# Performance work log

Measured on AMD Instinct MI355X. Metric: run time of the kernel, lower is better.

The kernel has to match this reference:

```python
import jax, jax.numpy as jnp
import numpy as np

N_NODES = 100000
N_EDGES = 1000000
HID = 128


def setup_inputs() -> dict:
    key = jax.random.key(0)
    ks = jax.random.split(key, 13)
    s = 0.05  # small init scale for numerical sanity
    return {
        "z": jax.random.normal(ks[0], (N_NODES, HID), jnp.float32),
        "edge": jax.random.randint(ks[1], (N_EDGES, 2), 0, N_NODES, jnp.int64),
        # hadamard_mlp: Linear(HID -> HID//2), ReLU, Linear(HID//2 -> 1)
        "w_h1": jax.random.normal(ks[2], (HID // 2, HID), jnp.float32) * s,
        "b_h1": jax.random.normal(ks[3], (HID // 2,), jnp.float32) * s,
        "w_h2": jax.random.normal(ks[4], (1, HID // 2), jnp.float32) * s,
        "b_h2": jax.random.normal(ks[5], (1,), jnp.float32) * s,
        # concat_mlp: Linear(2*HID -> HID), ReLU, Linear(HID -> 1)
        "w_c1": jax.random.normal(ks[6], (HID, 2 * HID), jnp.float32) * s,
        "b_c1": jax.random.normal(ks[7], (HID,), jnp.float32) * s,
        "w_c2": jax.random.normal(ks[8], (1, HID), jnp.float32) * s,
        "b_c2": jax.random.normal(ks[9], (1,), jnp.float32) * s,
        # bilinear: weight [1, HID, HID], bias [1]
        "w_b": jax.random.normal(ks[10], (1, HID, HID), jnp.float32) * s,
        "b_b": jax.random.normal(ks[11], (1,), jnp.float32) * s,
        "strategy_weights": jnp.ones((3,), jnp.float32) / 3.0,
    }


def reference(z, edge, w_h1, b_h1, w_h2, b_h2, w_c1, b_c1, w_c2, b_c2,
              w_b, b_b, strategy_weights):
    src, dst = edge[:, 0], edge[:, 1]
    z_src = z[src]                      # [E, D] gather
    z_dst = z[dst]                      # [E, D] gather
    w = jax.nn.softmax(strategy_weights)

    # strategy 1: hadamard MLP (dropout is identity in eval)
    had = z_src * z_dst                 # [E, D]
    h = jax.nn.relu(jnp.einsum('ed,hd->eh', had, w_h1) + b_h1)
    score1 = (jnp.einsum('eh,oh->eo', h, w_h2) + b_h2)[:, 0]

    # strategy 2: concat MLP
    cat = jnp.concatenate([z_src, z_dst], axis=1)  # [E, 2D]
    c = jax.nn.relu(jnp.einsum('ed,hd->eh', cat, w_c1) + b_c1)
    score2 = (jnp.einsum('eh,oh->eo', c, w_c2) + b_c2)[:, 0]

    # strategy 3: bilinear  out_e = z_src_e^T W z_dst_e + b
    score3 = jnp.einsum('ed,df,ef->e', z_src, w_b[0], z_dst) + b_b[0]

    return w[0] * score1 + w[1] * score2 + w[2] * score3
```

## Files before the change

### kernel.cpp

```cpp
#include <hip/hip_runtime.h>
#include <hip/hip_bf16.h>

#define N_NODES 100000
#define N_EDGES 1000000
#define SRCB 384
#define DSTB 512
#define NB (N_EDGES / 16)
#define NCHUNK (N_NODES / 16)

typedef float f32x4 __attribute__((ext_vector_type(4)));
typedef float f32x2 __attribute__((ext_vector_type(2)));
typedef _Float16 f16x8 __attribute__((ext_vector_type(8)));
typedef _Float16 f16x2 __attribute__((ext_vector_type(2)));

__device__ inline f16x8 pack8(float4 a, float4 b) {
    f16x8 o;
    o[0] = (_Float16)a.x; o[1] = (_Float16)a.y; o[2] = (_Float16)a.z; o[3] = (_Float16)a.w;
    o[4] = (_Float16)b.x; o[5] = (_Float16)b.y; o[6] = (_Float16)b.z; o[7] = (_Float16)b.w;
    return o;
}
__device__ inline void mfma16(f32x4& acc, f16x8 a, f16x8 b) {
    acc = __builtin_amdgcn_mfma_f32_16x16x32_f16(a, b, acc, 0, 0, 0);
}
__device__ inline float fdot2(f16x8 a, f16x8 b, int j2, float c) {
    f16x2 pa = { a[2 * j2], a[2 * j2 + 1] };
    f16x2 pb = { b[2 * j2], b[2 * j2 + 1] };
    return __builtin_amdgcn_fdot2(pa, pb, c, false);
}
__device__ inline unsigned char f2fp8(float v) {
    int p = __builtin_amdgcn_cvt_pk_fp8_f32(v, v, 0, false);
    return (unsigned char)(p & 0xff);
}

__global__ __launch_bounds__(512) void precomp_kernel(
    const float* __restrict__ z, const float* __restrict__ w_c1,
    const float* __restrict__ b_c1, const float* __restrict__ w_b,
    unsigned char* __restrict__ Ps8, unsigned char* __restrict__ Pd8)
{
    __shared__ f16x8 wlds[3072];

    const int tid = threadIdx.x;
    const int w = tid >> 6;
    const int lane = tid & 63;
    const int r = lane & 15, g = lane >> 4;
    const int gw = blockIdx.x * 8 + w;
    const int nW = gridDim.x * 8;

    float bc1v[2][4];
#pragma unroll
    for (int t = 0; t < 2; ++t)
#pragma unroll
        for (int nt = 0; nt < 4; ++nt)
            bc1v[t][nt] = b_c1[t * 64 + nt * 16 + r];

    for (int phase = 0; phase < 2; ++phase) {
        if (phase) __syncthreads();
        for (int i = tid; i < 3072; i += 512) {
            const int r_ = i & 15, g_ = (i >> 4) & 3, kk = (i >> 6) & 3;
            const int nt = (i >> 8) & 3, t = i >> 10;
            const int c = (phase * 3 + t) * 64 + nt * 16 + r_;
            const float* wrow;
            if (c < 128)       wrow = w_c1 + (size_t)c * 256;
            else if (c < 256)  wrow = w_c1 + (size_t)(c - 128) * 256 + 128;
            else               wrow = w_b + (size_t)(c - 256) * 128;
            const int k0 = kk * 32 + g_ * 8;
            float4 f0 = *reinterpret_cast<const float4*>(wrow + k0);
            float4 f1 = *reinterpret_cast<const float4*>(wrow + k0 + 4);
            wlds[i] = pack8(f0, f1);
        }
        __syncthreads();

        const f16x8* myw = wlds + g * 16 + r;

        for (int nb = gw; nb < NCHUNK; nb += nW) {
            const int node_r = nb * 16 + r;
            const float* zp = z + (size_t)node_r * 128;
            f16x8 a[4];
#pragma unroll
            for (int kk = 0; kk < 4; ++kk) {
                const int k0 = kk * 32 + g * 8;
                float4 z0 = *reinterpret_cast<const float4*>(zp + k0);
                float4 z1 = *reinterpret_cast<const float4*>(zp + k0 + 4);
                a[kk] = pack8(z0, z1);
                if (phase == 0) {
                    *reinterpret_cast<f16x8*>(
                        Ps8 + (size_t)node_r * SRCB + 128 + k0 * 2) = a[kk];
                    int q0 = __builtin_amdgcn_cvt_pk_fp8_f32(z0.x, z0.y, 0, false);
                    q0 = __builtin_amdgcn_cvt_pk_fp8_f32(z0.z, z0.w, q0, true);
                    int q1 = __builtin_amdgcn_cvt_pk_fp8_f32(z1.x, z1.y, 0, false);
                    q1 = __builtin_amdgcn_cvt_pk_fp8_f32(z1.z, z1.w, q1, true);
                    uint2 pk; pk.x = (unsigned)q0; pk.y = (unsigned)q1;
                    *reinterpret_cast<uint2*>(
                        Pd8 + (size_t)node_r * DSTB + 384 + k0) = pk;
                }
            }
#pragma unroll
            for (int t = 0; t < 3; ++t) {
                const int ct = phase * 3 + t;
                f32x4 acc[4] = {};
#pragma unroll
                for (int kk = 0; kk < 4; ++kk) {
#pragma unroll
                    for (int nt = 0; nt < 4; ++nt)
                        mfma16(acc[nt], a[kk], myw[((t * 4 + nt) * 4 + kk) * 64]);
                }
#pragma unroll
                for (int nt = 0; nt < 4; ++nt) {
#pragma unroll
                    for (int rr = 0; rr < 4; ++rr) {
                        const int node = nb * 16 + g * 4 + rr;
                        const int c = ct * 64 + nt * 16 + r;
                        float v = acc[nt][rr];
                        if (ct < 2) {
                            v += bc1v[ct][nt];
                            Ps8[(size_t)node * SRCB + c] = f2fp8(v);
                        } else if (ct < 4) {
                            Pd8[(size_t)node * DSTB + (c - 128)] = f2fp8(v);
                        } else {
                            *reinterpret_cast<_Float16*>(
                                Pd8 + (size_t)node * DSTB + 128
                                    + (size_t)(c - 256) * 2) = (_Float16)v;
                        }
                    }
                }
            }
        }
    }
}

__global__ __launch_bounds__(256) void edge_kernel(
    const int2* __restrict__ edge2,
    const unsigned char* __restrict__ Ps8, const unsigned char* __restrict__ Pd8,
    const float* __restrict__ w_h1, const float* __restrict__ b_h1,
    const float* __restrict__ w_h2, const float* __restrict__ b_h2,
    const float* __restrict__ w_c2, const float* __restrict__ b_c2,
    const float* __restrict__ b_b, const float* __restrict__ sw,
    float* __restrict__ out)
{
    __shared__ f16x8 bwlds[1024];

    const int tid = threadIdx.x;
    for (int e = tid; e < 1024; e += 256) {
        const int r_ = e & 15, g_ = (e >> 4) & 3, kkf = (e >> 6) & 3, ntf = e >> 8;
        const float* wr = w_h1 + (size_t)(ntf * 16 + r_) * 128 + g_ * 32 + kkf * 8;
        float4 f0 = *reinterpret_cast<const float4*>(wr);
        float4 f1 = *reinterpret_cast<const float4*>(wr + 4);
        bwlds[e] = pack8(f0, f1);
    }
    __syncthreads();

    const int lane = tid & 63;
    const int r = lane & 15, g = lane >> 4;

    const float s0 = sw[0], s1 = sw[1], s2 = sw[2];
    const float mx = fmaxf(s0, fmaxf(s1, s2));
    const float e0 = __expf(s0 - mx), e1 = __expf(s1 - mx), e2 = __expf(s2 - mx);
    const float inv = 1.0f / (e0 + e1 + e2);
    const float W0 = e0 * inv, W1 = e1 * inv, W2 = e2 * inv;
    const float cbias = W0 * b_h2[0] + W1 * b_c2[0] + W2 * b_b[0];

    float bh1v[4], wh2v[4];
#pragma unroll
    for (int nt = 0; nt < 4; ++nt) {
        bh1v[nt] = b_h1[nt * 16 + r];
        wh2v[nt] = w_h2[nt * 16 + r] * W0;
    }
    f16x8 wc2r[4];
#pragma unroll
    for (int kk = 0; kk < 4; ++kk) {
        const int k0 = g * 32 + kk * 8;
        float4 f0 = *reinterpret_cast<const float4*>(w_c2 + k0);
        float4 f1 = *reinterpret_cast<const float4*>(w_c2 + k0 + 4);
        f0.x *= W1; f0.y *= W1; f0.z *= W1; f0.w *= W1;
        f1.x *= W1; f1.y *= W1; f1.z *= W1; f1.w *= W1;
        wc2r[kk] = pack8(f0, f1);
    }
    const f16x8* myb = bwlds + g * 16 + r;

    const int gwid = (blockIdx.x * blockDim.x + tid) >> 6;
    const int nW = (gridDim.x * blockDim.x) >> 6;
    const int rsel = r & 3;
    const int srcl = ((r >> 2) << 4) | r;

    int b = gwid;
    int2 sd = make_int2(0, 0);
    if (b < NB) sd = edge2[b * 16 + r];

    for (; b < NB; b += nW) {
        const int bn = b + nW;
        int2 sdn = sd;
        if (bn < NB) sdn = edge2[bn * 16 + r];

        const int base = b * 16;
        const unsigned char* ps = Ps8 + (size_t)sd.x * SRCB;
        const unsigned char* pd = Pd8 + (size_t)sd.y * DSTB;

        uint4 a16[2], b16[2], zq[2];
        f16x8 zs[4], yv[4];
        a16[0] = *reinterpret_cast<const uint4*>(ps + g * 32);
        a16[1] = *reinterpret_cast<const uint4*>(ps + g * 32 + 16);
        b16[0] = *reinterpret_cast<const uint4*>(pd + g * 32);
        b16[1] = *reinterpret_cast<const uint4*>(pd + g * 32 + 16);
        zq[0]  = *reinterpret_cast<const uint4*>(pd + 384 + g * 32);
        zq[1]  = *reinterpret_cast<const uint4*>(pd + 384 + g * 32 + 16);
#pragma unroll
        for (int kk = 0; kk < 4; ++kk) {
            const int of = g * 64 + kk * 16;
            zs[kk] = *reinterpret_cast<const f16x8*>(ps + 128 + of);
            yv[kk] = *reinterpret_cast<const f16x8*>(pd + 128 + of);
        }
        const unsigned zdw[8] = { zq[0].x, zq[0].y, zq[0].z, zq[0].w,
                                  zq[1].x, zq[1].y, zq[1].z, zq[1].w };

        f32x4 acc[4] = {};
#pragma unroll
        for (int kk = 0; kk < 4; ++kk) {
            f32x2 p0 = __builtin_amdgcn_cvt_pk_f32_fp8((int)zdw[2 * kk], false);
            f32x2 p1 = __builtin_amdgcn_cvt_pk_f32_fp8((int)zdw[2 * kk], true);
            f32x2 p2 = __builtin_amdgcn_cvt_pk_f32_fp8((int)zdw[2 * kk + 1], false);
            f32x2 p3 = __builtin_amdgcn_cvt_pk_f32_fp8((int)zdw[2 * kk + 1], true);
            f16x8 a;
            a[0] = (_Float16)((float)zs[kk][0] * p0.x);
            a[1] = (_Float16)((float)zs[kk][1] * p0.y);
            a[2] = (_Float16)((float)zs[kk][2] * p1.x);
            a[3] = (_Float16)((float)zs[kk][3] * p1.y);
            a[4] = (_Float16)((float)zs[kk][4] * p2.x);
            a[5] = (_Float16)((float)zs[kk][5] * p2.y);
            a[6] = (_Float16)((float)zs[kk][6] * p3.x);
            a[7] = (_Float16)((float)zs[kk][7] * p3.y);
            mfma16(acc[0], a, myb[(0 * 4 + kk) * 64]);
            mfma16(acc[1], a, myb[(1 * 4 + kk) * 64]);
            mfma16(acc[2], a, myb[(2 * 4 + kk) * 64]);
            mfma16(acc[3], a, myb[(3 * 4 + kk) * 64]);
        }
        float t4[4];
#pragma unroll
        for (int rr = 0; rr < 4; ++rr) {
            float s = 0.f;
#pragma unroll
            for (int nt = 0; nt < 4; ++nt)
                s = fmaf(fmaxf(acc[nt][rr] + bh1v[nt], 0.f), wh2v[nt], s);
            t4[rr] = s;
        }
#pragma unroll
        for (int mask = 1; mask <= 8; mask <<= 1) {
#pragma unroll
            for (int rr = 0; rr < 4; ++rr)
                t4[rr] += __shfl_xor(t4[rr], mask, 16);
        }
        float u = t4[0];
        if (rsel == 1) u = t4[1];
        if (rsel == 2) u = t4[2];
        if (rsel == 3) u = t4[3];
        const float sc1w = __shfl(u, srcl, 64);

        float sA = 0.f, sB = 0.f;
#pragma unroll
        for (int h = 0; h < 2; ++h) {
            const unsigned ax = a16[h].x, ay = a16[h].y, az = a16[h].z, aw = a16[h].w;
            const unsigned bx = b16[h].x, by = b16[h].y, bz = b16[h].z, bw_ = b16[h].w;
            f32x2 pa0 = __builtin_amdgcn_cvt_pk_f32_fp8((int)ax, false);
            f32x2 pa1 = __builtin_amdgcn_cvt_pk_f32_fp8((int)ax, true);
            f32x2 pa2 = __builtin_amdgcn_cvt_pk_f32_fp8((int)ay, false);
            f32x2 pa3 = __builtin_amdgcn_cvt_pk_f32_fp8((int)ay, true);
            f32x2 pa4 = __builtin_amdgcn_cvt_pk_f32_fp8((int)az, false);
            f32x2 pa5 = __builtin_amdgcn_cvt_pk_f32_fp8((int)az, true);
            f32x2 pa6 = __builtin_amdgcn_cvt_pk_f32_fp8((int)aw, false);
            f32x2 pa7 = __builtin_amdgcn_cvt_pk_f32_fp8((int)aw, true);
            f32x2 pb0 = __builtin_amdgcn_cvt_pk_f32_fp8((int)bx, false);
            f32x2 pb1 = __builtin_amdgcn_cvt_pk_f32_fp8((int)bx, true);
            f32x2 pb2 = __builtin_amdgcn_cvt_pk_f32_fp8((int)by, false);
            f32x2 pb3 = __builtin_amdgcn_cvt_pk_f32_fp8((int)by, true);
            f32x2 pb4 = __builtin_amdgcn_cvt_pk_f32_fp8((int)bz, false);
            f32x2 pb5 = __builtin_amdgcn_cvt_pk_f32_fp8((int)bz, true);
            f32x2 pb6 = __builtin_amdgcn_cvt_pk_f32_fp8((int)bw_, false);
            f32x2 pb7 = __builtin_amdgcn_cvt_pk_f32_fp8((int)bw_, true);
            const f16x8 w0 = wc2r[2 * h], w1 = wc2r[2 * h + 1];
            sA = fmaf(fmaxf(pa0.x + pb0.x, 0.f), (float)w0[0], sA);
            sA = fmaf(fmaxf(pa0.y + pb0.y, 0.f), (float)w0[1], sA);
            sA = fmaf(fmaxf(pa1.x + pb1.x, 0.f), (float)w0[2], sA);
            sA = fmaf(fmaxf(pa1.y + pb1.y, 0.f), (float)w0[3], sA);
            sA = fmaf(fmaxf(pa2.x + pb2.x, 0.f), (float)w0[4], sA);
            sA = fmaf(fmaxf(pa2.y + pb2.y, 0.f), (float)w0[5], sA);
            sA = fmaf(fmaxf(pa3.x + pb3.x, 0.f), (float)w0[6], sA);
            sA = fmaf(fmaxf(pa3.y + pb3.y, 0.f), (float)w0[7], sA);
            sA = fmaf(fmaxf(pa4.x + pb4.x, 0.f), (float)w1[0], sA);
            sA = fmaf(fmaxf(pa4.y + pb4.y, 0.f), (float)w1[1], sA);
            sA = fmaf(fmaxf(pa5.x + pb5.x, 0.f), (float)w1[2], sA);
            sA = fmaf(fmaxf(pa5.y + pb5.y, 0.f), (float)w1[3], sA);
            sA = fmaf(fmaxf(pa6.x + pb6.x, 0.f), (float)w1[4], sA);
            sA = fmaf(fmaxf(pa6.y + pb6.y, 0.f), (float)w1[5], sA);
            sA = fmaf(fmaxf(pa7.x + pb7.x, 0.f), (float)w1[6], sA);
            sA = fmaf(fmaxf(pa7.y + pb7.y, 0.f), (float)w1[7], sA);
        }
#pragma unroll
        for (int kk = 0; kk < 4; ++kk)
#pragma unroll
            for (int j2 = 0; j2 < 4; ++j2)
                sB = fdot2(zs[kk], yv[kk], j2, sB);

        sA += __shfl_xor(sA, 16, 64);
        sA += __shfl_xor(sA, 32, 64);
        sB += __shfl_xor(sB, 16, 64);
        sB += __shfl_xor(sB, 32, 64);

        const float res = sc1w + sA + fmaf(W2, sB, cbias);
        if (lane < 16) out[base + lane] = res;
        sd = sdn;
    }
}

__global__ __launch_bounds__(256) void fused_fallback(
    const float* __restrict__ z, const int* __restrict__ edge,
    const float* __restrict__ w_h1, const float* __restrict__ b_h1,
    const float* __restrict__ w_h2, const float* __restrict__ b_h2,
    const float* __restrict__ w_c1, const float* __restrict__ b_c1,
    const float* __restrict__ w_c2, const float* __restrict__ b_c2,
    const float* __restrict__ w_b, const float* __restrict__ b_b,
    const float* __restrict__ sw, float* __restrict__ out)
{
    __shared__ float zbuf[4][256];
    const int lane = threadIdx.x & 63;
    const int w = threadIdx.x >> 6;
    const int gw = blockIdx.x * 4 + w;
    const int nw = gridDim.x * 4;

    const float s0 = sw[0], s1 = sw[1], s2 = sw[2];
    const float mx = fmaxf(s0, fmaxf(s1, s2));
    const float e0 = __expf(s0 - mx), e1 = __expf(s1 - mx), e2 = __expf(s2 - mx);
    const float inv = 1.0f / (e0 + e1 + e2);
    const float W0 = e0 * inv, W1 = e1 * inv, W2 = e2 * inv;
    const float cbias = W0 * b_h2[0] + W1 * b_c2[0] + W2 * b_b[0];

    for (int e = gw; e < N_EDGES; e += nw) {
        const int src = edge[2 * e], dst = edge[2 * e + 1];
        const float zs0 = z[(size_t)src * 128 + lane];
        const float zs1 = z[(size_t)src * 128 + 64 + lane];
        const float zd0 = z[(size_t)dst * 128 + lane];
        const float zd1 = z[(size_t)dst * 128 + 64 + lane];
        zbuf[w][lane] = zs0; zbuf[w][64 + lane] = zs1;
        zbuf[w][128 + lane] = zd0; zbuf[w][192 + lane] = zd1;
        asm volatile("s_waitcnt lgkmcnt(0)" ::: "memory");

        float h = 0.f;
        const float* whr = w_h1 + (size_t)lane * 128;
        for (int d = 0; d < 128; ++d)
            h = fmaf(zbuf[w][d] * zbuf[w][128 + d], whr[d], h);
        float sc1 = fmaxf(h + b_h1[lane], 0.f) * w_h2[lane];

        float c0 = 0.f, c1 = 0.f;
        const float* w0r = w_c1 + (size_t)lane * 256;
        const float* w1r = w_c1 + (size_t)(lane + 64) * 256;
        for (int d = 0; d < 256; ++d) {
            const float cat = zbuf[w][d];
            c0 = fmaf(cat, w0r[d], c0);
            c1 = fmaf(cat, w1r[d], c1);
        }
        float sc2 = fmaxf(c0 + b_c1[lane], 0.f) * w_c2[lane]
                  + fmaxf(c1 + b_c1[lane + 64], 0.f) * w_c2[lane + 64];

        float t0 = 0.f, t1 = 0.f;
        const float* wb0 = w_b + (size_t)lane * 128;
        const float* wb1 = w_b + (size_t)(lane + 64) * 128;
        for (int f = 0; f < 128; ++f) {
            const float zdf = zbuf[w][128 + f];
            t0 = fmaf(wb0[f], zdf, t0);
            t1 = fmaf(wb1[f], zdf, t1);
        }
        float sc3 = zs0 * t0 + zs1 * t1;

        float v = fmaf(W0, sc1, fmaf(W1, sc2, W2 * sc3));
#pragma unroll
        for (int m = 1; m < 64; m <<= 1) v += __shfl_xor(v, m, 64);
        if (lane == 0) out[e] = v + cbias;
    }
}

extern "C" void kernel_launch(void* const* d_in, const int* in_sizes, int n_in,
                              void* d_out, int out_size, void* d_ws, size_t ws_size,
                              hipStream_t stream)
{
    const float* z    = (const float*)d_in[0];
    const int*   edge = (const int*)d_in[1];
    const float* w_h1 = (const float*)d_in[2];
    const float* b_h1 = (const float*)d_in[3];
    const float* w_h2 = (const float*)d_in[4];
    const float* b_h2 = (const float*)d_in[5];
    const float* w_c1 = (const float*)d_in[6];
    const float* b_c1 = (const float*)d_in[7];
    const float* w_c2 = (const float*)d_in[8];
    const float* b_c2 = (const float*)d_in[9];
    const float* w_b  = (const float*)d_in[10];
    const float* b_b  = (const float*)d_in[11];
    const float* sw   = (const float*)d_in[12];
    float* outp = (float*)d_out;

    const size_t szSrc = (size_t)N_NODES * SRCB;
    const size_t szDst = (size_t)N_NODES * DSTB;
    const size_t need  = szSrc + szDst;

    if (ws_size >= need) {
        unsigned char* Ps8 = (unsigned char*)d_ws;
        unsigned char* Pd8 = (unsigned char*)d_ws + szSrc;
        hipLaunchKernelGGL(precomp_kernel, dim3(512), dim3(512), 0, stream,
                           z, w_c1, b_c1, w_b, Ps8, Pd8);
        hipLaunchKernelGGL(edge_kernel, dim3(1024), dim3(256), 0, stream,
                           (const int2*)edge, Ps8, Pd8, w_h1, b_h1, w_h2, b_h2,
                           w_c2, b_c2, b_b, sw, outp);
    } else {
        hipLaunchKernelGGL(fused_fallback, dim3(4096), dim3(256), 0, stream,
                           z, edge, w_h1, b_h1, w_h2, b_h2, w_c1, b_c1,
                           w_c2, b_c2, w_b, b_b, sw, outp);
    }
}
```

Baseline: 188.7 us.

## Merge precompute phases and use fp8 MFMA for concat-MLP projections

The precompute kernel previously made two passes over all nodes, reloading z and swapping the weight set in LDS between passes. It now keeps both weight sets resident in LDS at once and processes every node in a single pass, halving the z reads. The concat-MLP first-layer projections now use fp8 weights and fp8 MFMA, while the bilinear projection stays in fp16. This cuts global traffic and MFMA cost in the precompute stage but adds quantization error to the concat projections.

```diff
diff --git a/kernel.cpp b/kernel.cpp
--- a/kernel.cpp
+++ b/kernel.cpp
@@ -19,8 +19,18 @@
     o[4] = (_Float16)b.x; o[5] = (_Float16)b.y; o[6] = (_Float16)b.z; o[7] = (_Float16)b.w;
     return o;
 }
+__device__ inline unsigned long long pkfp8x8(float4 a, float4 b) {
+    int q0 = __builtin_amdgcn_cvt_pk_fp8_f32(a.x, a.y, 0, false);
+    q0 = __builtin_amdgcn_cvt_pk_fp8_f32(a.z, a.w, q0, true);
+    int q1 = __builtin_amdgcn_cvt_pk_fp8_f32(b.x, b.y, 0, false);
+    q1 = __builtin_amdgcn_cvt_pk_fp8_f32(b.z, b.w, q1, true);
+    return ((unsigned long long)(unsigned)q1 << 32) | (unsigned)q0;
+}
 __device__ inline void mfma16(f32x4& acc, f16x8 a, f16x8 b) {
     acc = __builtin_amdgcn_mfma_f32_16x16x32_f16(a, b, acc, 0, 0, 0);
+}
+__device__ inline void mfma8(f32x4& acc, long a, long b) {
+    acc = __builtin_amdgcn_mfma_f32_16x16x32_fp8_fp8(a, b, acc, 0, 0, 0);
 }
 __device__ inline float fdot2(f16x8 a, f16x8 b, int j2, float c) {
     f16x2 pa = { a[2 * j2], a[2 * j2 + 1] };
@@ -37,7 +47,8 @@
     const float* __restrict__ b_c1, const float* __restrict__ w_b,
     unsigned char* __restrict__ Ps8, unsigned char* __restrict__ Pd8)
 {
-    __shared__ f16x8 wlds[3072];
+    __shared__ unsigned long long w8[4096];
+    __shared__ f16x8 w16[2048];
 
     const int tid = threadIdx.x;
     const int w = tid >> 6;
@@ -53,75 +64,93 @@
         for (int nt = 0; nt < 4; ++nt)
             bc1v[t][nt] = b_c1[t * 64 + nt * 16 + r];
 
-    for (int phase = 0; phase < 2; ++phase) {
-        if (phase) __syncthreads();
-        for (int i = tid; i < 3072; i += 512) {
-            const int r_ = i & 15, g_ = (i >> 4) & 3, kk = (i >> 6) & 3;
-            const int nt = (i >> 8) & 3, t = i >> 10;
-            const int c = (phase * 3 + t) * 64 + nt * 16 + r_;
-            const float* wrow;
-            if (c < 128)       wrow = w_c1 + (size_t)c * 256;
-            else if (c < 256)  wrow = w_c1 + (size_t)(c - 128) * 256 + 128;
-            else               wrow = w_b + (size_t)(c - 256) * 128;
-            const int k0 = kk * 32 + g_ * 8;
-            float4 f0 = *reinterpret_cast<const float4*>(wrow + k0);
-            float4 f1 = *reinterpret_cast<const float4*>(wrow + k0 + 4);
-            wlds[i] = pack8(f0, f1);
-        }
-        __syncthreads();
-
-        const f16x8* myw = wlds + g * 16 + r;
-
-        for (int nb = gw; nb < NCHUNK; nb += nW) {
-            const int node_r = nb * 16 + r;
-            const float* zp = z + (size_t)node_r * 128;
-            f16x8 a[4];
+    for (int i = tid; i < 4096; i += 512) {
+        const int r_ = i & 15, g_ = (i >> 4) & 3, kk = (i >> 6) & 3;
+        const int nt = (i >> 8) & 3, t = i >> 10;
+        const int c = t * 64 + nt * 16 + r_;
+        const float* wrow = (c < 128) ? (w_c1 + (size_t)c * 256)
+                                      : (w_c1 + (size_t)(c - 128) * 256 + 128);
+        const int k0 = kk * 32 + g_ * 8;
+        float4 f0 = *reinterpret_cast<const float4*>(wrow + k0);
+        float4 f1 = *reinterpret_cast<const float4*>(wrow + k0 + 4);
+        w8[i] = pkfp8x8(f0, f1);
+    }
+    for (int i = tid; i < 2048; i += 512) {
+        const int r_ = i & 15, g_ = (i >> 4) & 3, kk = (i >> 6) & 3;
+        const int nt = (i >> 8) & 3, t = i >> 10;
+        const int c = (4 + t) * 64 + nt * 16 + r_;
+        const float* wrow = w_b + (size_t)(c - 256) * 128;
+        const int k0 = kk * 32 + g_ * 8;
+        float4 f0 = *reinterpret_cast<const float4*>(wrow + k0);
+        float4 f1 = *reinterpret_cast<const float4*>(wrow + k0 + 4);
+        w16[i] = pack8(f0, f1);
+    }
+    __syncthreads();
+
+    const unsigned long long* myw8 = w8 + g * 16 + r;
+    const f16x8* myw16 = w16 + g * 16 + r;
+
+    for (int nb = gw; nb < NCHUNK; nb += nW) {
+        const int node_r = nb * 16 + r;
+        const float* zp = z + (size_t)node_r * 128;
+        f16x8 a16[4];
+        unsigned long long a8[4];
+#pragma unroll
+        for (int kk = 0; kk < 4; ++kk) {
+            const int k0 = kk * 32 + g * 8;
+            float4 z0 = *reinterpret_cast<const float4*>(zp + k0);
+            float4 z1 = *reinterpret_cast<const float4*>(zp + k0 + 4);
+            a16[kk] = pack8(z0, z1);
+            a8[kk] = pkfp8x8(z0, z1);
+            *reinterpret_cast<f16x8*>(
+                Ps8 + (size_t)node_r * SRCB + 128 + k0 * 2) = a16[kk];
+            *reinterpret_cast<unsigned long long*>(
+                Pd8 + (size_t)node_r * DSTB + 384 + k0) = a8[kk];
+        }
+#pragma unroll
+        for (int t = 0; t < 4; ++t) {
+            f32x4 acc[4] = {};
 #pragma unroll
             for (int kk = 0; kk < 4; ++kk) {
-                const int k0 = kk * 32 + g * 8;
-                float4 z0 = *reinterpret_cast<const float4*>(zp + k0);
-                float4 z1 = *reinterpret_cast<const float4*>(zp + k0 + 4);
-                a[kk] = pack8(z0, z1);
-                if (phase == 0) {
-                    *reinterpret_cast<f16x8*>(
-                        Ps8 + (size_t)node_r * SRCB + 128 + k0 * 2) = a[kk];
-                    int q0 = __builtin_amdgcn_cvt_pk_fp8_f32(z0.x, z0.y, 0, false);
-                    q0 = __builtin_amdgcn_cvt_pk_fp8_f32(z0.z, z0.w, q0, true);
-                    int q1 = __builtin_amdgcn_cvt_pk_fp8_f32(z1.x, z1.y, 0, false);
-                    q1 = __builtin_amdgcn_cvt_pk_fp8_f32(z1.z, z1.w, q1, true);
-                    uint2 pk; pk.x = (unsigned)q0; pk.y = (unsigned)q1;
-                    *reinterpret_cast<uint2*>(
-                        Pd8 + (size_t)node_r * DSTB + 384 + k0) = pk;
+#pragma unroll
+                for (int nt = 0; nt < 4; ++nt)
+                    mfma8(acc[nt], (long)a8[kk],
+                          (long)myw8[((t * 4 + nt) * 4 + kk) * 64]);
+            }
+#pragma unroll
+            for (int nt = 0; nt < 4; ++nt) {
+#pragma unroll
+                for (int rr = 0; rr < 4; ++rr) {
+                    const int node = nb * 16 + g * 4 + rr;
+                    const int c = t * 64 + nt * 16 + r;
+                    float v = acc[nt][rr];
+                    if (t < 2) {
+                        v += bc1v[t][nt];
+                        Ps8[(size_t)node * SRCB + c] = f2fp8(v);
+                    } else {
+                        Pd8[(size_t)node * DSTB + (c - 128)] = f2fp8(v);
+                    }
                 }
             }
-#pragma unroll
-            for (int t = 0; t < 3; ++t) {
-                const int ct = phase * 3 + t;
-                f32x4 acc[4] = {};
-#pragma unroll
-                for (int kk = 0; kk < 4; ++kk) {
-#pragma unroll
-                    for (int nt = 0; nt < 4; ++nt)
-                        mfma16(acc[nt], a[kk], myw[((t * 4 + nt) * 4 + kk) * 64]);
-                }
-#pragma unroll
-                for (int nt = 0; nt < 4; ++nt) {
-#pragma unroll
-                    for (int rr = 0; rr < 4; ++rr) {
-                        const int node = nb * 16 + g * 4 + rr;
-                        const int c = ct * 64 + nt * 16 + r;
-                        float v = acc[nt][rr];
-                        if (ct < 2) {
-                            v += bc1v[ct][nt];
-                            Ps8[(size_t)node * SRCB + c] = f2fp8(v);
-                        } else if (ct < 4) {
-                            Pd8[(size_t)node * DSTB + (c - 128)] = f2fp8(v);
-                        } else {
-                            *reinterpret_cast<_Float16*>(
-                                Pd8 + (size_t)node * DSTB + 128
-                                    + (size_t)(c - 256) * 2) = (_Float16)v;
-                        }
-                    }
+        }
+#pragma unroll
+        for (int t = 0; t < 2; ++t) {
+            f32x4 acc[4] = {};
+#pragma unroll
+            for (int kk = 0; kk < 4; ++kk) {
+#pragma unroll
+                for (int nt = 0; nt < 4; ++nt)
+                    mfma16(acc[nt], a16[kk], myw16[((t * 4 + nt) * 4 + kk) * 64]);
+            }
+#pragma unroll
+            for (int nt = 0; nt < 4; ++nt) {
+#pragma unroll
+                for (int rr = 0; rr < 4; ++rr) {
+                    const int node = nb * 16 + g * 4 + rr;
+                    const int c = (4 + t) * 64 + nt * 16 + r;
+                    *reinterpret_cast<_Float16*>(
+                        Pd8 + (size_t)node * DSTB + 128
+                            + (size_t)(c - 256) * 2) = (_Float16)acc[nt][rr];
                 }
             }
         }
```

After: 178.7 us. 5.3% less time.
